# Performance work log

Measured on AMD Instinct MI355X. Metric: run time of the kernel, lower is better.

## Reference

```python
import jax, jax.numpy as jnp
import numpy as np

N = 50000      # nodes
E = 800000     # edges
D_IN = 128     # input feature dim
HID = 64       # out_channels (per-head dim; concat=False -> head mean)
HEADS = 2
NEG_SLOPE = 0.2


def gat_layer(x, src, dst, Ws, Wd, a_s, a_d, b):
    # PyG GATConv, add_self_loops=False, concat=False (mean over heads)
    n = x.shape[0]
    H, C = a_s.shape
    hs = (x @ Ws).reshape(n, H, C)          # source-side features [N,H,C]
    hd = (x @ Wd).reshape(n, H, C)          # dest-side features   [N,H,C]
    als = (hs * a_s).sum(-1)                # [N,H]
    ald = (hd * a_d).sum(-1)                # [N,H]
    e = jax.nn.leaky_relu(als[src] + ald[dst], NEG_SLOPE)   # [E,H]
    # segment softmax over edges grouped by destination node
    m = jax.ops.segment_max(e, dst, num_segments=n)
    m = jax.lax.stop_gradient(jnp.where(jnp.isfinite(m), m, 0.0))
    ex = jnp.exp(e - m[dst])
    den = jax.ops.segment_sum(ex, dst, num_segments=n)
    alpha = ex / (den[dst] + 1e-16)                          # [E,H]
    out = jax.ops.segment_sum(hs[src] * alpha[:, :, None], dst, num_segments=n)
    return out.mean(axis=1) + b             # [N,C]


def setup_inputs() -> dict:
    key = jax.random.key(0)
    ks = jax.random.split(key, 32)
    d = {}
    d["x"] = jax.random.normal(ks[0], (N, D_IN), jnp.float32)
    d["edge_index"] = jax.random.randint(ks[1], (2, E), 0, N, jnp.int32)
    dins = [D_IN, HID, HID]
    i = 2
    for l in range(1, 4):
        din = dins[l - 1]
        s = 1.0 / np.sqrt(din)
        d[f"Ws{l}"] = jax.random.normal(ks[i], (din, HEADS * HID), jnp.float32) * s; i += 1
        d[f"Wd{l}"] = jax.random.normal(ks[i], (din, HEADS * HID), jnp.float32) * s; i += 1
        d[f"as{l}"] = jax.random.normal(ks[i], (HEADS, HID), jnp.float32) * 0.1; i += 1
        d[f"ad{l}"] = jax.random.normal(ks[i], (HEADS, HID), jnp.float32) * 0.1; i += 1
        d[f"b{l}"] = jnp.zeros((HID,), jnp.float32)
        d[f"Wl{l}"] = jax.random.normal(ks[i], (din, HID), jnp.float32) * s; i += 1
        d[f"bl{l}"] = jnp.zeros((HID,), jnp.float32)
    return d


def reference(x, edge_index,
              Ws1, Wd1, as1, ad1, b1, Wl1, bl1,
              Ws2, Wd2, as2, ad2, b2, Wl2, bl2,
              Ws3, Wd3, as3, ad3, b3, Wl3, bl3):
    src, dst = edge_index[0], edge_index[1]
    h = jax.nn.relu(gat_layer(x, src, dst, Ws1, Wd1, as1, ad1, b1) + x @ Wl1 + bl1)
    h = jax.nn.relu(gat_layer(h, src, dst, Ws2, Wd2, as2, ad2, b2) + h @ Wl2 + bl2)
    h = jax.nn.relu(gat_layer(h, src, dst, Ws3, Wd3, as3, ad3, b3) + h @ Wl3 + bl3)
    return h
```

## Files before the change

kernel.cpp:

```cpp
#include <hip/hip_runtime.h>
#include <hip/hip_bf16.h>

#define NN 50000
#define NE 800000
#define SCAN_BS 1024
#define SCAN_NB ((NN + SCAN_BS - 1) / SCAN_BS)
#define EB ((NE + 255) / 256)
#define GB ((NN + 63) / 64)
#define RB ((NN + 1 + 255) / 256)

typedef __attribute__((ext_vector_type(8))) __bf16 bf16x8;
typedef __attribute__((ext_vector_type(4))) float float4v;

__device__ __forceinline__ unsigned pack_bf2(float lo, float hi) {
    union { __bf16 b; unsigned short u; } a, c;
    a.b = (__bf16)lo; c.b = (__bf16)hi;
    return (unsigned)a.u | ((unsigned)c.u << 16);
}
__device__ __forceinline__ float2 unpack_bf2(unsigned v) {
    union { unsigned short u; __bf16 b; } lo, hi;
    lo.u = (unsigned short)(v & 0xffff); hi.u = (unsigned short)(v >> 16);
    return make_float2((float)lo.b, (float)hi.b);
}


__device__ __forceinline__ void convert_w_part(const float* __restrict__ Ws,
                                               const float* __restrict__ Wd,
                                               const float* __restrict__ Wl,
                                               __bf16* __restrict__ Wt, int K, int i)
{
    if (i >= 320 * K) return;
    int c = i / K, k = i % K;
    float v;
    if (c < 128)      v = Ws[k * 128 + c];
    else if (c < 256) v = Wd[k * 128 + (c - 128)];
    else              v = Wl[k * 64 + (c - 256)];
    Wt[i] = (__bf16)v;
}

__global__ void __launch_bounds__(256)
prep_kernel(const int* __restrict__ ei, int* __restrict__ deg, int* __restrict__ rank,
            const float* __restrict__ Ws1, const float* __restrict__ Wd1,
            const float* __restrict__ Wl1, __bf16* __restrict__ Wt1,
            const float* __restrict__ Ws2, const float* __restrict__ Wd2,
            const float* __restrict__ Wl2, __bf16* __restrict__ Wt2,
            const float* __restrict__ Ws3, const float* __restrict__ Wd3,
            const float* __restrict__ Wl3, __bf16* __restrict__ Wt3)
{
    int bi = blockIdx.x;
    if (bi < EB) {
        int e = bi * 256 + threadIdx.x;
        if (e < NE) rank[e] = atomicAdd(&deg[ei[NE + e]], 1);
    } else if (bi < EB + 160) {
        convert_w_part(Ws1, Wd1, Wl1, Wt1, 128, (bi - EB) * 256 + threadIdx.x);
    } else if (bi < EB + 240) {
        convert_w_part(Ws2, Wd2, Wl2, Wt2, 64, (bi - EB - 160) * 256 + threadIdx.x);
    } else {
        convert_w_part(Ws3, Wd3, Wl3, Wt3, 64, (bi - EB - 240) * 256 + threadIdx.x);
    }
}


__global__ void __launch_bounds__(SCAN_BS)
scan12_kernel(const int* __restrict__ deg, int* __restrict__ exl,
              int* __restrict__ bsum, int* __restrict__ boff, int* __restrict__ ticket)
{
    __shared__ int sh[SCAN_BS];
    __shared__ int lastFlag;
    int t = threadIdx.x;
    int i = blockIdx.x * SCAN_BS + t;
    int v = (i < NN) ? deg[i] : 0;
    sh[t] = v;
    __syncthreads();
    for (int off = 1; off < SCAN_BS; off <<= 1) {
        int u = (t >= off) ? sh[t - off] : 0;
        __syncthreads();
        sh[t] += u;
        __syncthreads();
    }
    if (i < NN) exl[i] = sh[t] - v;
    if (t == SCAN_BS - 1) {
        bsum[blockIdx.x] = sh[t];
        __threadfence();
        lastFlag = (atomicAdd(ticket, 1) == SCAN_NB - 1);
    }
    __syncthreads();
    if (lastFlag && t < 64) {
        __threadfence();
        int l = t;
        int bv = (l < SCAN_NB) ? bsum[l] : 0;
        int own = bv;
        for (int off = 1; off < 64; off <<= 1) {
            int u = __shfl_up(bv, off);
            if (l >= off) bv += u;
        }
        if (l < SCAN_NB) boff[l] = bv - own;
    }
}


__device__ __forceinline__ bf16x8 load_af(const __bf16* p) { return *(const bf16x8*)p; }
__device__ __forceinline__ bf16x8 load_af(const float* p) {
    float4 u = *(const float4*)p;
    float4 v = *(const float4*)(p + 4);
    bf16x8 r;
    r[0] = (__bf16)u.x; r[1] = (__bf16)u.y; r[2] = (__bf16)u.z; r[3] = (__bf16)u.w;
    r[4] = (__bf16)v.x; r[5] = (__bf16)v.y; r[6] = (__bf16)v.z; r[7] = (__bf16)v.w;
    return r;
}

template <int K, typename TIN, bool FUSE>
__global__ void __launch_bounds__(256)
mfma_gemm(const TIN* __restrict__ xin, const __bf16* __restrict__ Wt,
          const float* __restrict__ a_s, const float* __restrict__ a_d,
          unsigned* __restrict__ hsb, float* __restrict__ lin,
          float* __restrict__ als, float* __restrict__ ald,
          const int* __restrict__ ei, const int* __restrict__ rank,
          const int* __restrict__ exl, const int* __restrict__ boff,
          int* __restrict__ row, int* __restrict__ csr_src)
{
    const int tid = threadIdx.x;

    if (FUSE && blockIdx.x >= GB) {
        int bi = blockIdx.x - GB;
        if (bi < RB) {
            int i = bi * 256 + tid;
            if (i < NN)       row[i] = exl[i] + boff[i >> 10];
            else if (i == NN) row[i] = NE;
        } else {
            int e = (bi - RB) * 256 + tid;
            if (e < NE) {
                int s = ei[e], d = ei[NE + e];
                csr_src[exl[d] + boff[d >> 10] + rank[e]] = s;
            }
        }
        return;
    }

    __shared__ __align__(16) char ldsE[2 * 64 * 68 * 4 + 1024];

    const int lane = tid & 63;
    const int wave = tid >> 6;
    const int l15 = lane & 15, quad = lane >> 4;
    const int nblk0 = blockIdx.x * 64;
    const int n0 = nblk0 + wave * 16;
    const int nA = min(n0 + l15, NN - 1);

    bf16x8 afr[K / 32];
#pragma unroll
    for (int ks = 0; ks < K / 32; ++ks)
        afr[ks] = load_af(xin + (size_t)nA * K + ks * 32 + quad * 8);

    float4v acc[20];
#pragma unroll
    for (int t = 0; t < 20; ++t) acc[t] = (float4v){0.f, 0.f, 0.f, 0.f};

    const __bf16* bp = Wt + (size_t)l15 * K + quad * 8;
#pragma unroll
    for (int ks = 0; ks < K / 32; ++ks) {
#pragma unroll
        for (int t = 0; t < 20; ++t) {
            bf16x8 bf = *(const bf16x8*)(bp + (size_t)t * 16 * K + ks * 32);
            acc[t] = __builtin_amdgcn_mfma_f32_16x16x32_bf16(afr[ks], bf, acc[t], 0, 0, 0);
        }
    }

    float s0[4], s1[4], d0[4], d1[4];
#pragma unroll
    for (int r = 0; r < 4; ++r) { s0[r] = 0.f; s1[r] = 0.f; d0[r] = 0.f; d1[r] = 0.f; }
#pragma unroll
    for (int t = 0; t < 4; ++t) {
        float as0 = a_s[t * 16 + l15];
        float as1 = a_s[64 + t * 16 + l15];
        float ad0 = a_d[t * 16 + l15];
        float ad1 = a_d[64 + t * 16 + l15];
#pragma unroll
        for (int r = 0; r < 4; ++r) {
            s0[r] += acc[t][r] * as0;
            s1[r] += acc[t + 4][r] * as1;
            d0[r] += acc[t + 8][r] * ad0;
            d1[r] += acc[t + 12][r] * ad1;
        }
    }
#pragma unroll
    for (int m = 1; m < 16; m <<= 1) {
#pragma unroll
        for (int r = 0; r < 4; ++r) {
            s0[r] += __shfl_xor(s0[r], m);
            s1[r] += __shfl_xor(s1[r], m);
            d0[r] += __shfl_xor(d0[r], m);
            d1[r] += __shfl_xor(d1[r], m);
        }
    }

    unsigned* hs_l  = (unsigned*)ldsE;
    float*    lin_l = (float*)(ldsE + 64 * 68 * 4);
    float*    al_l  = (float*)(ldsE + 2 * 64 * 68 * 4);

#pragma unroll
    for (int t = 0; t < 4; ++t) {
#pragma unroll
        for (int r = 0; r < 4; ++r) {
            int ln = wave * 16 + quad * 4 + r;
            hs_l[ln * 68 + t * 16 + l15] = pack_bf2(acc[t][r], acc[t + 4][r]);
            lin_l[ln * 68 + t * 16 + l15] = acc[t + 16][r];
        }
    }
    if (l15 == 0) {
#pragma unroll
        for (int r = 0; r < 4; ++r) {
            int ln = wave * 16 + quad * 4 + r;
            al_l[0 * 64 + ln] = s0[r];
            al_l[1 * 64 + ln] = s1[r];
            al_l[2 * 64 + ln] = d0[r];
            al_l[3 * 64 + ln] = d1[r];
        }
    }
    __syncthreads();

#pragma unroll
    for (int it = 0; it < 4; ++it) {
        int idx4 = it * 256 + tid;
        int ln = idx4 >> 4, c4 = idx4 & 15;
        int n = nblk0 + ln;
        if (n < NN) {
            *(uint4*)&hsb[(size_t)n * 64 + c4 * 4] =
                *(const uint4*)&hs_l[ln * 68 + c4 * 4];
            *(float4*)&lin[(size_t)n * 64 + c4 * 4] =
                *(const float4*)&lin_l[ln * 68 + c4 * 4];
        }
    }
    {
        int half = tid >> 7;
        int t2 = tid & 127;
        int ln = t2 >> 1, h = t2 & 1;
        int n = nblk0 + ln;
        if (n < NN) {
            float v = al_l[(half * 2 + h) * 64 + ln];
            if (half == 0) als[n * 2 + h] = v;
            else           ald[n * 2 + h] = v;
        }
    }
}


__device__ __forceinline__ float2 edge_w(const float* __restrict__ als, int s,
                                         float ad0, float ad1)
{
    float2 al = *(const float2*)&als[s * 2];
    float e0 = al.x + ad0; e0 = (e0 >= 0.f) ? e0 : 0.2f * e0;
    float e1 = al.y + ad1; e1 = (e1 >= 0.f) ? e1 : 0.2f * e1;
    return make_float2(__expf(e0), __expf(e1));
}

__device__ __forceinline__ void store_q(float* p, float v0, float v1, float v2, float v3) {
    *(float4*)p = make_float4(v0, v1, v2, v3);
}
__device__ __forceinline__ void store_q(__bf16* p, float v0, float v1, float v2, float v3) {
    *(uint2*)p = make_uint2(pack_bf2(v0, v1), pack_bf2(v2, v3));
}

template <typename TO>
__global__ void __launch_bounds__(256)
gat_aggregate(const int* __restrict__ row, const int* __restrict__ csr_src,
              const float* __restrict__ als, const float* __restrict__ ald,
              const unsigned* __restrict__ hsb, const float* __restrict__ lin,
              const float* __restrict__ b, const float* __restrict__ bl,
              TO* __restrict__ out)
{
    int w = (blockIdx.x * 256 + threadIdx.x) >> 6;
    int lane = threadIdx.x & 63;
    int q = lane >> 4;
    int l15 = lane & 15;
    if (w >= NN) return;
    int p0 = row[w], p1 = row[w + 1];
    float ad0 = ald[w * 2 + 0];
    float ad1 = ald[w * 2 + 1];

    float a0[4] = {0.f, 0.f, 0.f, 0.f};
    float a1[4] = {0.f, 0.f, 0.f, 0.f};
    float den0 = 0.f, den1 = 0.f;

    int p = p0 + q;
    for (; p + 12 < p1; p += 16) {
        int sA = csr_src[p];
        int sB = csr_src[p + 4];
        int sC = csr_src[p + 8];
        int sD = csr_src[p + 12];
        float2 eA = edge_w(als, sA, ad0, ad1);
        float2 eB = edge_w(als, sB, ad0, ad1);
        float2 eC = edge_w(als, sC, ad0, ad1);
        float2 eD = edge_w(als, sD, ad0, ad1);
        uint4 gA = *(const uint4*)&hsb[(size_t)sA * 64 + 4 * l15];
        uint4 gB = *(const uint4*)&hsb[(size_t)sB * 64 + 4 * l15];
        uint4 gC = *(const uint4*)&hsb[(size_t)sC * 64 + 4 * l15];
        uint4 gD = *(const uint4*)&hsb[(size_t)sD * 64 + 4 * l15];
        den0 += (eA.x + eB.x) + (eC.x + eD.x);
        den1 += (eA.y + eB.y) + (eC.y + eD.y);
        float2 h;
        h = unpack_bf2(gA.x); a0[0] += eA.x * h.x; a1[0] += eA.y * h.y;
        h = unpack_bf2(gA.y); a0[1] += eA.x * h.x; a1[1] += eA.y * h.y;
        h = unpack_bf2(gA.z); a0[2] += eA.x * h.x; a1[2] += eA.y * h.y;
        h = unpack_bf2(gA.w); a0[3] += eA.x * h.x; a1[3] += eA.y * h.y;
        h = unpack_bf2(gB.x); a0[0] += eB.x * h.x; a1[0] += eB.y * h.y;
        h = unpack_bf2(gB.y); a0[1] += eB.x * h.x; a1[1] += eB.y * h.y;
        h = unpack_bf2(gB.z); a0[2] += eB.x * h.x; a1[2] += eB.y * h.y;
        h = unpack_bf2(gB.w); a0[3] += eB.x * h.x; a1[3] += eB.y * h.y;
        h = unpack_bf2(gC.x); a0[0] += eC.x * h.x; a1[0] += eC.y * h.y;
        h = unpack_bf2(gC.y); a0[1] += eC.x * h.x; a1[1] += eC.y * h.y;
        h = unpack_bf2(gC.z); a0[2] += eC.x * h.x; a1[2] += eC.y * h.y;
        h = unpack_bf2(gC.w); a0[3] += eC.x * h.x; a1[3] += eC.y * h.y;
        h = unpack_bf2(gD.x); a0[0] += eD.x * h.x; a1[0] += eD.y * h.y;
        h = unpack_bf2(gD.y); a0[1] += eD.x * h.x; a1[1] += eD.y * h.y;
        h = unpack_bf2(gD.z); a0[2] += eD.x * h.x; a1[2] += eD.y * h.y;
        h = unpack_bf2(gD.w); a0[3] += eD.x * h.x; a1[3] += eD.y * h.y;
    }
    for (; p + 4 < p1; p += 8) {
        int sA = csr_src[p];
        int sB = csr_src[p + 4];
        float2 eA = edge_w(als, sA, ad0, ad1);
        float2 eB = edge_w(als, sB, ad0, ad1);
        uint4 gA = *(const uint4*)&hsb[(size_t)sA * 64 + 4 * l15];
        uint4 gB = *(const uint4*)&hsb[(size_t)sB * 64 + 4 * l15];
        den0 += eA.x + eB.x;
        den1 += eA.y + eB.y;
        float2 h;
        h = unpack_bf2(gA.x); a0[0] += eA.x * h.x; a1[0] += eA.y * h.y;
        h = unpack_bf2(gA.y); a0[1] += eA.x * h.x; a1[1] += eA.y * h.y;
        h = unpack_bf2(gA.z); a0[2] += eA.x * h.x; a1[2] += eA.y * h.y;
        h = unpack_bf2(gA.w); a0[3] += eA.x * h.x; a1[3] += eA.y * h.y;
        h = unpack_bf2(gB.x); a0[0] += eB.x * h.x; a1[0] += eB.y * h.y;
        h = unpack_bf2(gB.y); a0[1] += eB.x * h.x; a1[1] += eB.y * h.y;
        h = unpack_bf2(gB.z); a0[2] += eB.x * h.x; a1[2] += eB.y * h.y;
        h = unpack_bf2(gB.w); a0[3] += eB.x * h.x; a1[3] += eB.y * h.y;
    }
    for (; p < p1; p += 4) {
        int s = csr_src[p];
        float2 e = edge_w(als, s, ad0, ad1);
        uint4 g = *(const uint4*)&hsb[(size_t)s * 64 + 4 * l15];
        den0 += e.x; den1 += e.y;
        float2 h;
        h = unpack_bf2(g.x); a0[0] += e.x * h.x; a1[0] += e.y * h.y;
        h = unpack_bf2(g.y); a0[1] += e.x * h.x; a1[1] += e.y * h.y;
        h = unpack_bf2(g.z); a0[2] += e.x * h.x; a1[2] += e.y * h.y;
        h = unpack_bf2(g.w); a0[3] += e.x * h.x; a1[3] += e.y * h.y;
    }

#pragma unroll
    for (int i = 0; i < 4; ++i) {
        a0[i] += __shfl_xor(a0[i], 16); a0[i] += __shfl_xor(a0[i], 32);
        a1[i] += __shfl_xor(a1[i], 16); a1[i] += __shfl_xor(a1[i], 32);
    }
    den0 += __shfl_xor(den0, 16); den0 += __shfl_xor(den0, 32);
    den1 += __shfl_xor(den1, 16); den1 += __shfl_xor(den1, 32);

    if (q == 0) {
        int c0 = 4 * l15;
        float r0 = 1.f / (den0 + 1e-16f);
        float r1 = 1.f / (den1 + 1e-16f);
        float4 lv = *(const float4*)&lin[(size_t)w * 64 + c0];
        float v0 = 0.5f * (a0[0] * r0 + a1[0] * r1) + b[c0 + 0] + bl[c0 + 0] + lv.x;
        float v1 = 0.5f * (a0[1] * r0 + a1[1] * r1) + b[c0 + 1] + bl[c0 + 1] + lv.y;
        float v2 = 0.5f * (a0[2] * r0 + a1[2] * r1) + b[c0 + 2] + bl[c0 + 2] + lv.z;
        float v3 = 0.5f * (a0[3] * r0 + a1[3] * r1) + b[c0 + 3] + bl[c0 + 3] + lv.w;
        store_q(&out[(size_t)w * 64 + c0],
                fmaxf(v0, 0.f), fmaxf(v1, 0.f), fmaxf(v2, 0.f), fmaxf(v3, 0.f));
    }
}


extern "C" void kernel_launch(void* const* d_in, const int* in_sizes, int n_in,
                              void* d_out, int out_size, void* d_ws, size_t ws_size,
                              hipStream_t stream)
{
    const float* x  = (const float*)d_in[0];
    const int*   ei = (const int*)d_in[1];
    const float* Ws[3]; const float* Wd[3]; const float* As[3]; const float* Ad[3];
    const float* Bb[3]; const float* Wl[3]; const float* Bl[3];
    for (int l = 0; l < 3; ++l) {
        int base = 2 + 7 * l;
        Ws[l] = (const float*)d_in[base + 0];
        Wd[l] = (const float*)d_in[base + 1];
        As[l] = (const float*)d_in[base + 2];
        Ad[l] = (const float*)d_in[base + 3];
        Bb[l] = (const float*)d_in[base + 4];
        Wl[l] = (const float*)d_in[base + 5];
        Bl[l] = (const float*)d_in[base + 6];
    }

    float* ws = (float*)d_ws;
    unsigned* hsb = (unsigned*)ws;
    float* lin  = (float*)(hsb + (size_t)NN * 64);
    float* als  = lin + (size_t)NN * 64;
    float* ald  = als + (size_t)NN * 2;
    __bf16* hb  = (__bf16*)(ald + (size_t)NN * 2);
    __bf16* Wt1 = hb + (size_t)NN * 64;
    __bf16* Wt2 = Wt1 + 320 * 128;
    __bf16* Wt3 = Wt2 + 320 * 64;
    int* row     = (int*)(Wt3 + 320 * 64);
    int* deg     = row + (NN + 1);
    int* ticket  = deg + NN;
    int* rank    = ticket + 1;
    int* exl     = rank + NE;
    int* bsum    = exl + NN;
    int* boff    = bsum + SCAN_NB;
    int* csr_src = boff + SCAN_NB;

    const int WB = (NN * 64 + 255) / 256;

    hipMemsetAsync(deg, 0, sizeof(int) * (NN + 1), stream);
    prep_kernel<<<EB + 320, 256, 0, stream>>>(ei, deg, rank,
        Ws[0], Wd[0], Wl[0], Wt1,
        Ws[1], Wd[1], Wl[1], Wt2,
        Ws[2], Wd[2], Wl[2], Wt3);
    scan12_kernel<<<SCAN_NB, SCAN_BS, 0, stream>>>(deg, exl, bsum, boff, ticket);

    for (int l = 0; l < 3; ++l) {
        if (l == 0) {
            mfma_gemm<128, float, true><<<GB + RB + EB, 256, 0, stream>>>(
                x, Wt1, As[0], Ad[0], hsb, lin, als, ald,
                ei, rank, exl, boff, row, csr_src);
        } else {
            const __bf16* wt = (l == 1) ? Wt2 : Wt3;
            mfma_gemm<64, __bf16, false><<<GB, 256, 0, stream>>>(
                hb, wt, As[l], Ad[l], hsb, lin, als, ald,
                nullptr, nullptr, nullptr, nullptr, nullptr, nullptr);
        }
        if (l == 2) {
            gat_aggregate<float><<<WB, 256, 0, stream>>>(
                row, csr_src, als, ald, hsb, lin, Bb[l], Bl[l], (float*)d_out);
        } else {
            gat_aggregate<__bf16><<<WB, 256, 0, stream>>>(
                row, csr_src, als, ald, hsb, lin, Bb[l], Bl[l], hb);
        }
    }
}
```

Measured before the change: 367.1 us.

## Stage GEMM weights in padded LDS tiles and swap MFMA operands for direct stores

Weights are pre-converted into padded 64-wide K chunks (row stride 72) that each GEMM block copies into LDS, with the second chunk prefetched into registers while the first is consumed. The MFMA operands are swapped so each lane holds four consecutive output columns of one node, which lets results and attention logits be written straight to global memory without the LDS transpose pass. CSR finishing is split back out of the first GEMM into its own kernel. The cost is extra LDS traffic, more barriers, one more launch, and a larger shared-memory footprint that may lower occupancy.

```diff
diff --git a/kernel.cpp b/kernel.cpp
--- a/kernel.cpp
+++ b/kernel.cpp
@@ -27,14 +27,18 @@
 __device__ __forceinline__ void convert_w_part(const float* __restrict__ Ws,
                                                const float* __restrict__ Wd,
                                                const float* __restrict__ Wl,
-                                               __bf16* __restrict__ Wt, int K, int i)
-{
-    if (i >= 320 * K) return;
-    int c = i / K, k = i % K;
-    float v;
-    if (c < 128)      v = Ws[k * 128 + c];
-    else if (c < 256) v = Wd[k * 128 + (c - 128)];
-    else              v = Wl[k * 64 + (c - 256)];
+                                               __bf16* __restrict__ Wt, int NC, int i)
+{
+    if (i >= NC * 23040) return;
+    int chunk = i / 23040, rem = i % 23040;
+    int r = rem / 72, c = rem % 72;
+    float v = 0.f;
+    if (c < 64) {
+        int k = chunk * 64 + c;
+        if (r < 128)      v = Ws[k * 128 + r];
+        else if (r < 256) v = Wd[k * 128 + (r - 128)];
+        else              v = Wl[k * 64 + (r - 256)];
+    }
     Wt[i] = (__bf16)v;
 }
 
@@ -51,12 +55,12 @@
     if (bi < EB) {
         int e = bi * 256 + threadIdx.x;
         if (e < NE) rank[e] = atomicAdd(&deg[ei[NE + e]], 1);
-    } else if (bi < EB + 160) {
-        convert_w_part(Ws1, Wd1, Wl1, Wt1, 128, (bi - EB) * 256 + threadIdx.x);
-    } else if (bi < EB + 240) {
-        convert_w_part(Ws2, Wd2, Wl2, Wt2, 64, (bi - EB - 160) * 256 + threadIdx.x);
+    } else if (bi < EB + 180) {
+        convert_w_part(Ws1, Wd1, Wl1, Wt1, 2, (bi - EB) * 256 + threadIdx.x);
+    } else if (bi < EB + 270) {
+        convert_w_part(Ws2, Wd2, Wl2, Wt2, 1, (bi - EB - 180) * 256 + threadIdx.x);
     } else {
-        convert_w_part(Ws3, Wd3, Wl3, Wt3, 64, (bi - EB - 240) * 256 + threadIdx.x);
+        convert_w_part(Ws3, Wd3, Wl3, Wt3, 1, (bi - EB - 270) * 256 + threadIdx.x);
     }
 }
 
@@ -99,6 +103,26 @@
 }
 
 
+__global__ void __launch_bounds__(256)
+csr_finish(const int* __restrict__ ei, const int* __restrict__ rank,
+           const int* __restrict__ exl, const int* __restrict__ boff,
+           int* __restrict__ row, int* __restrict__ csr_src)
+{
+    int bi = blockIdx.x;
+    if (bi < RB) {
+        int i = bi * 256 + threadIdx.x;
+        if (i < NN)       row[i] = exl[i] + boff[i >> 10];
+        else if (i == NN) row[i] = NE;
+    } else {
+        int e = (bi - RB) * 256 + threadIdx.x;
+        if (e < NE) {
+            int s = ei[e], d = ei[NE + e];
+            csr_src[exl[d] + boff[d >> 10] + rank[e]] = s;
+        }
+    }
+}
+
+
 __device__ __forceinline__ bf16x8 load_af(const __bf16* p) { return *(const bf16x8*)p; }
 __device__ __forceinline__ bf16x8 load_af(const float* p) {
     float4 u = *(const float4*)p;
@@ -109,41 +133,21 @@
     return r;
 }
 
-template <int K, typename TIN, bool FUSE>
+template <int K, typename TIN>
 __global__ void __launch_bounds__(256)
 mfma_gemm(const TIN* __restrict__ xin, const __bf16* __restrict__ Wt,
           const float* __restrict__ a_s, const float* __restrict__ a_d,
           unsigned* __restrict__ hsb, float* __restrict__ lin,
-          float* __restrict__ als, float* __restrict__ ald,
-          const int* __restrict__ ei, const int* __restrict__ rank,
-          const int* __restrict__ exl, const int* __restrict__ boff,
-          int* __restrict__ row, int* __restrict__ csr_src)
-{
-    const int tid = threadIdx.x;
-
-    if (FUSE && blockIdx.x >= GB) {
-        int bi = blockIdx.x - GB;
-        if (bi < RB) {
-            int i = bi * 256 + tid;
-            if (i < NN)       row[i] = exl[i] + boff[i >> 10];
-            else if (i == NN) row[i] = NE;
-        } else {
-            int e = (bi - RB) * 256 + tid;
-            if (e < NE) {
-                int s = ei[e], d = ei[NE + e];
-                csr_src[exl[d] + boff[d >> 10] + rank[e]] = s;
-            }
-        }
-        return;
-    }
-
-    __shared__ __align__(16) char ldsE[2 * 64 * 68 * 4 + 1024];
-
+          float* __restrict__ als, float* __restrict__ ald)
+{
+    constexpr int NC = K / 64;
+    __shared__ __align__(16) char ldsW[320 * 144];
+
+    const int tid  = threadIdx.x;
     const int lane = tid & 63;
     const int wave = tid >> 6;
     const int l15 = lane & 15, quad = lane >> 4;
-    const int nblk0 = blockIdx.x * 64;
-    const int n0 = nblk0 + wave * 16;
+    const int n0 = blockIdx.x * 64 + wave * 16;
     const int nA = min(n0 + l15, NN - 1);
 
     bf16x8 afr[K / 32];
@@ -151,95 +155,82 @@
     for (int ks = 0; ks < K / 32; ++ks)
         afr[ks] = load_af(xin + (size_t)nA * K + ks * 32 + quad * 8);
 
+    const uint4* gW = (const uint4*)Wt;
+    uint4* lw = (uint4*)ldsW;
+    uint4 st[12];
+
+#pragma unroll
+    for (int i = 0; i < 12; ++i) { int idx = i * 256 + tid; if (idx < 2880) st[i] = gW[idx]; }
+
     float4v acc[20];
 #pragma unroll
     for (int t = 0; t < 20; ++t) acc[t] = (float4v){0.f, 0.f, 0.f, 0.f};
 
-    const __bf16* bp = Wt + (size_t)l15 * K + quad * 8;
-#pragma unroll
-    for (int ks = 0; ks < K / 32; ++ks) {
+#pragma unroll
+    for (int i = 0; i < 12; ++i) { int idx = i * 256 + tid; if (idx < 2880) lw[idx] = st[i]; }
+    __syncthreads();
+
+    if constexpr (NC == 2) {
+#pragma unroll
+        for (int i = 0; i < 12; ++i) { int idx = i * 256 + tid; if (idx < 2880) st[i] = gW[2880 + idx]; }
+    }
+
+#pragma unroll
+    for (int ksh = 0; ksh < 2; ++ksh) {
 #pragma unroll
         for (int t = 0; t < 20; ++t) {
-            bf16x8 bf = *(const bf16x8*)(bp + (size_t)t * 16 * K + ks * 32);
-            acc[t] = __builtin_amdgcn_mfma_f32_16x16x32_bf16(afr[ks], bf, acc[t], 0, 0, 0);
-        }
-    }
-
-    float s0[4], s1[4], d0[4], d1[4];
-#pragma unroll
-    for (int r = 0; r < 4; ++r) { s0[r] = 0.f; s1[r] = 0.f; d0[r] = 0.f; d1[r] = 0.f; }
+            bf16x8 bw = *(const bf16x8*)&ldsW[(t * 16 + l15) * 144 + (ksh * 4 + quad) * 16];
+            acc[t] = __builtin_amdgcn_mfma_f32_16x16x32_bf16(bw, afr[ksh], acc[t], 0, 0, 0);
+        }
+    }
+
+    if constexpr (NC == 2) {
+        __syncthreads();
+#pragma unroll
+        for (int i = 0; i < 12; ++i) { int idx = i * 256 + tid; if (idx < 2880) lw[idx] = st[i]; }
+        __syncthreads();
+#pragma unroll
+        for (int ksh = 0; ksh < 2; ++ksh) {
+#pragma unroll
+            for (int t = 0; t < 20; ++t) {
+                bf16x8 bw = *(const bf16x8*)&ldsW[(t * 16 + l15) * 144 + (ksh * 4 + quad) * 16];
+                acc[t] = __builtin_amdgcn_mfma_f32_16x16x32_bf16(bw, afr[2 + ksh], acc[t], 0, 0, 0);
+            }
+        }
+    }
+
+    float s0 = 0.f, s1 = 0.f, d0 = 0.f, d1 = 0.f;
 #pragma unroll
     for (int t = 0; t < 4; ++t) {
-        float as0 = a_s[t * 16 + l15];
-        float as1 = a_s[64 + t * 16 + l15];
-        float ad0 = a_d[t * 16 + l15];
-        float ad1 = a_d[64 + t * 16 + l15];
-#pragma unroll
-        for (int r = 0; r < 4; ++r) {
-            s0[r] += acc[t][r] * as0;
-            s1[r] += acc[t + 4][r] * as1;
-            d0[r] += acc[t + 8][r] * ad0;
-            d1[r] += acc[t + 12][r] * ad1;
-        }
-    }
-#pragma unroll
-    for (int m = 1; m < 16; m <<= 1) {
-#pragma unroll
-        for (int r = 0; r < 4; ++r) {
-            s0[r] += __shfl_xor(s0[r], m);
-            s1[r] += __shfl_xor(s1[r], m);
-            d0[r] += __shfl_xor(d0[r], m);
-            d1[r] += __shfl_xor(d1[r], m);
-        }
-    }
-
-    unsigned* hs_l  = (unsigned*)ldsE;
-    float*    lin_l = (float*)(ldsE + 64 * 68 * 4);
-    float*    al_l  = (float*)(ldsE + 2 * 64 * 68 * 4);
-
-#pragma unroll
-    for (int t = 0; t < 4; ++t) {
-#pragma unroll
-        for (int r = 0; r < 4; ++r) {
-            int ln = wave * 16 + quad * 4 + r;
-            hs_l[ln * 68 + t * 16 + l15] = pack_bf2(acc[t][r], acc[t + 4][r]);
-            lin_l[ln * 68 + t * 16 + l15] = acc[t + 16][r];
-        }
-    }
-    if (l15 == 0) {
-#pragma unroll
-        for (int r = 0; r < 4; ++r) {
-            int ln = wave * 16 + quad * 4 + r;
-            al_l[0 * 64 + ln] = s0[r];
-            al_l[1 * 64 + ln] = s1[r];
-            al_l[2 * 64 + ln] = d0[r];
-            al_l[3 * 64 + ln] = d1[r];
-        }
-    }
-    __syncthreads();
-
-#pragma unroll
-    for (int it = 0; it < 4; ++it) {
-        int idx4 = it * 256 + tid;
-        int ln = idx4 >> 4, c4 = idx4 & 15;
-        int n = nblk0 + ln;
-        if (n < NN) {
-            *(uint4*)&hsb[(size_t)n * 64 + c4 * 4] =
-                *(const uint4*)&hs_l[ln * 68 + c4 * 4];
-            *(float4*)&lin[(size_t)n * 64 + c4 * 4] =
-                *(const float4*)&lin_l[ln * 68 + c4 * 4];
-        }
-    }
-    {
-        int half = tid >> 7;
-        int t2 = tid & 127;
-        int ln = t2 >> 1, h = t2 & 1;
-        int n = nblk0 + ln;
-        if (n < NN) {
-            float v = al_l[(half * 2 + h) * 64 + ln];
-            if (half == 0) als[n * 2 + h] = v;
-            else           ald[n * 2 + h] = v;
-        }
+        float4 as0 = *(const float4*)&a_s[t * 16 + quad * 4];
+        float4 as1 = *(const float4*)&a_s[64 + t * 16 + quad * 4];
+        float4 ad0 = *(const float4*)&a_d[t * 16 + quad * 4];
+        float4 ad1 = *(const float4*)&a_d[64 + t * 16 + quad * 4];
+        s0 += acc[t][0] * as0.x + acc[t][1] * as0.y + acc[t][2] * as0.z + acc[t][3] * as0.w;
+        s1 += acc[t + 4][0] * as1.x + acc[t + 4][1] * as1.y + acc[t + 4][2] * as1.z + acc[t + 4][3] * as1.w;
+        d0 += acc[t + 8][0] * ad0.x + acc[t + 8][1] * ad0.y + acc[t + 8][2] * ad0.z + acc[t + 8][3] * ad0.w;
+        d1 += acc[t + 12][0] * ad1.x + acc[t + 12][1] * ad1.y + acc[t + 12][2] * ad1.z + acc[t + 12][3] * ad1.w;
+    }
+    s0 += __shfl_xor(s0, 16); s0 += __shfl_xor(s0, 32);
+    s1 += __shfl_xor(s1, 16); s1 += __shfl_xor(s1, 32);
+    d0 += __shfl_xor(d0, 16); d0 += __shfl_xor(d0, 32);
+    d1 += __shfl_xor(d1, 16); d1 += __shfl_xor(d1, 32);
+
+    int n = n0 + l15;
+    if (n < NN) {
+#pragma unroll
+        for (int t = 0; t < 4; ++t) {
+            uint4 u;
+            u.x = pack_bf2(acc[t][0], acc[t + 4][0]);
+            u.y = pack_bf2(acc[t][1], acc[t + 4][1]);
+            u.z = pack_bf2(acc[t][2], acc[t + 4][2]);
+            u.w = pack_bf2(acc[t][3], acc[t + 4][3]);
+            *(uint4*)&hsb[(size_t)n * 64 + t * 16 + quad * 4] = u;
+            *(float4*)&lin[(size_t)n * 64 + t * 16 + quad * 4] =
+                make_float4(acc[16 + t][0], acc[16 + t][1], acc[16 + t][2], acc[16 + t][3]);
+        }
+        if (quad == 0) *(float2*)&als[(size_t)n * 2] = make_float2(s0, s1);
+        if (quad == 1) *(float2*)&ald[(size_t)n * 2] = make_float2(d0, d1);
     }
 }
 
@@ -395,9 +386,9 @@
     float* ald  = als + (size_t)NN * 2;
     __bf16* hb  = (__bf16*)(ald + (size_t)NN * 2);
     __bf16* Wt1 = hb + (size_t)NN * 64;
-    __bf16* Wt2 = Wt1 + 320 * 128;
-    __bf16* Wt3 = Wt2 + 320 * 64;
-    int* row     = (int*)(Wt3 + 320 * 64);
+    __bf16* Wt2 = Wt1 + 2 * 320 * 72;
+    __bf16* Wt3 = Wt2 + 320 * 72;
+    int* row     = (int*)(Wt3 + 320 * 72);
     int* deg     = row + (NN + 1);
     int* ticket  = deg + NN;
     int* rank    = ticket + 1;
@@ -409,22 +400,21 @@
     const int WB = (NN * 64 + 255) / 256;
 
     hipMemsetAsync(deg, 0, sizeof(int) * (NN + 1), stream);
-    prep_kernel<<<EB + 320, 256, 0, stream>>>(ei, deg, rank,
+    prep_kernel<<<EB + 360, 256, 0, stream>>>(ei, deg, rank,
         Ws[0], Wd[0], Wl[0], Wt1,
         Ws[1], Wd[1], Wl[1], Wt2,
         Ws[2], Wd[2], Wl[2], Wt3);
     scan12_kernel<<<SCAN_NB, SCAN_BS, 0, stream>>>(deg, exl, bsum, boff, ticket);
+    csr_finish<<<RB + EB, 256, 0, stream>>>(ei, rank, exl, boff, row, csr_src);
 
     for (int l = 0; l < 3; ++l) {
         if (l == 0) {
-            mfma_gemm<128, float, true><<<GB + RB + EB, 256, 0, stream>>>(
-                x, Wt1, As[0], Ad[0], hsb, lin, als, ald,
-                ei, rank, exl, boff, row, csr_src);
+            mfma_gemm<128, float><<<GB, 256, 0, stream>>>(
+                x, Wt1, As[0], Ad[0], hsb, lin, als, ald);
         } else {
             const __bf16* wt = (l == 1) ? Wt2 : Wt3;
-            mfma_gemm<64, __bf16, false><<<GB, 256, 0, stream>>>(
-                hb, wt, As[l], Ad[l], hsb, lin, als, ald,
-                nullptr, nullptr, nullptr, nullptr, nullptr, nullptr);
+            mfma_gemm<64, __bf16><<<GB, 256, 0, stream>>>(
+                hb, wt, As[l], Ad[l], hsb, lin, als, ald);
         }
         if (l == 2) {
             gat_aggregate<float><<<WB, 256, 0, stream>>>(
```

After: 363.8 us. No clear change (-0.9%).
